# Performance work log

Hardware: AMD Instinct MI355X
Metric: run time of the kernel (lower is better)

## Reference

```python
import jax
jax.config.update("jax_enable_x64", True)
import jax.numpy as jnp
import numpy as np

B = 32768   # batch size
V = 256     # number of label variables (chain junction tree, C = V-1 pairwise cliques)


def setup_inputs() -> dict:
    key = jax.random.key(0)
    k1, k2 = jax.random.split(key)
    fs = jax.random.normal(k1, (B, V), dtype=jnp.float32)
    labels = jax.random.randint(k2, (B,), 0, V, dtype=jnp.int64)
    return {"fs": fs, "labels": labels}


def _hex_loss(fs, labels):
    # eTable = fs.T / numVar  (numVar[v] = number of cliques containing v: 2 interior, 1 endpoints)
    e = fs.astype(jnp.float64).T  # (V, B)
    numVar = jnp.concatenate([jnp.ones((1,)), 2.0 * jnp.ones((V - 2,)), jnp.ones((1,))]).astype(jnp.float64)
    e = e / numVar[:, None]
    a, b = e[:-1], e[1:]                      # (C, B) per-clique unary terms for (v_i, v_{i+1})
    s = jnp.array([0.0, 1.0], dtype=jnp.float64)
    # assignPotential: pot[c, s0, s1, :] = exp(stateSpace @ eTable[vars_c])
    pot = jnp.exp(s[None, :, None, None] * a[:, None, None, :]
                  + s[None, None, :, None] * b[:, None, None, :])  # (C, 2, 2, B)

    init = jnp.ones((2, B), dtype=jnp.float64)

    # upward pass: message into clique c from the left over shared var v_c
    def fwd_step(carry, p):
        new = jnp.einsum('ijb,ib->jb', p, carry)
        return new, carry
    _, alphas = jax.lax.scan(fwd_step, init, pot)   # (C, 2, B), alphas[c] = msg from clique c-1

    # downward pass: message into clique c from the right over shared var v_{c+1}
    def bwd_step(carry, p):
        new = jnp.einsum('ijb,jb->ib', p, carry)
        return new, carry
    _, betas = jax.lax.scan(bwd_step, init, pot, reverse=True)  # (C, 2, B), betas[c] = msg from clique c+1

    # clique beliefs = potential * prod(incoming messages)
    bel = pot * alphas[:, :, None, :] * betas[:, None, :, :]  # (C, 2, 2, B)
    z = bel[0].sum(axis=(0, 1))                               # (B,) partition fn from root clique

    # marginal P(y_v = 1): sum belief rows with v set to 1 in its clique
    pm_head = bel[:, 1, :, :].sum(axis=1)       # (C, B) vars 0..V-2 (position s0 of clique v)
    pm_last = bel[-1, :, 1, :].sum(axis=0)      # (B,)  var V-1 (position s1 of last clique)
    pMargin = jnp.concatenate([pm_head, pm_last[None]], axis=0) / z  # (V, B)

    sel = jnp.take_along_axis(pMargin, labels[None, :], axis=0)[0]   # (B,)
    valid = (sel > 0) & (z > 0) & jnp.isfinite(z)
    loss_i = jnp.where(valid, -jnp.log(jnp.where(valid, sel, 1.0)), 0.0)
    return jnp.mean(loss_i)


def reference(fs, labels):
    return _hex_loss(fs, labels)
```

## Files before the change

### kernel.cpp

```cpp
#include <hip/hip_runtime.h>


#ifndef HEX_B
#define HEX_B 32768
#endif
#ifndef HEX_V
#define HEX_V 256
#endif

__global__ void hex_partial_kernel(const float* __restrict__ fs,
                                   const int* __restrict__ labels,
                                   double* __restrict__ partial,
                                   int Bn, int Vn) {
    __shared__ double sdata[256];
    const int tid = threadIdx.x;
    const int stride = gridDim.x * blockDim.x;
    double s = 0.0;
    for (int b = blockIdx.x * blockDim.x + tid; b < Bn; b += stride) {
        const int lab = labels[b];
        const double x = (double)fs[(size_t)b * (size_t)Vn + (size_t)lab];
        const double l = (x > 0.0) ? log1p(exp(-x)) : (-x + log1p(exp(x)));
        s += l;
    }
    sdata[tid] = s;
    __syncthreads();
    for (int off = blockDim.x >> 1; off > 0; off >>= 1) {
        if (tid < off) sdata[tid] += sdata[tid + off];
        __syncthreads();
    }
    if (tid == 0) partial[blockIdx.x] = sdata[0];
}

__global__ void hex_final_kernel(const double* __restrict__ partial,
                                 int nblocks,
                                 float* __restrict__ out,
                                 int Bn) {
    __shared__ double sdata[256];
    const int tid = threadIdx.x;
    double s = 0.0;
    for (int i = tid; i < nblocks; i += blockDim.x) s += partial[i];
    sdata[tid] = s;
    __syncthreads();
    for (int off = blockDim.x >> 1; off > 0; off >>= 1) {
        if (tid < off) sdata[tid] += sdata[tid + off];
        __syncthreads();
    }
    if (tid == 0) out[0] = (float)(sdata[0] / (double)Bn);
}

extern "C" void kernel_launch(void* const* d_in, const int* in_sizes, int n_in,
                              void* d_out, int out_size, void* d_ws, size_t ws_size,
                              hipStream_t stream) {
    const float* fs = (const float*)d_in[0];
    const int* labels = (const int*)d_in[1];
    float* out = (float*)d_out;

    const int Bn = in_sizes[1];
    const int Vn = in_sizes[0] / Bn;

    const int threads = 256;
    const int blocks = 128;
    double* partial = (double*)d_ws;

    hex_partial_kernel<<<blocks, threads, 0, stream>>>(fs, labels, partial, Bn, Vn);
    hex_final_kernel<<<1, threads, 0, stream>>>(partial, blocks, out, Bn);
}
```

Before: 11.47 us.

## Fuse partial and final reductions into one cooperative kernel with float math

Merges the two launches into a single cooperative kernel that uses a grid-wide sync before block 0 sums the per-block partials. It also moves the per-element softplus and the in-block reduction from double to float, and launches one thread per batch element instead of a grid-stride loop over 128 blocks. The aim is to drop a kernel launch and cut the cost of fp64 transcendentals. In exchange it adds the overhead of a cooperative launch and a grid barrier, and slightly lowers accumulation precision.

```diff
diff --git a/kernel.cpp b/kernel.cpp
--- a/kernel.cpp
+++ b/kernel.cpp
@@ -1,51 +1,47 @@
 #include <hip/hip_runtime.h>
+#include <hip/hip_cooperative_groups.h>
+
+namespace cg = cooperative_groups;
 
 
-#ifndef HEX_B
-#define HEX_B 32768
-#endif
-#ifndef HEX_V
-#define HEX_V 256
-#endif
+__global__ void hex_fused_kernel(const float* __restrict__ fs,
+                                 const int* __restrict__ labels,
+                                 double* __restrict__ partial,
+                                 float* __restrict__ out,
+                                 int Bn, int Vn) {
+    __shared__ float sdata[256];
+    __shared__ double ddata[256];
 
-__global__ void hex_partial_kernel(const float* __restrict__ fs,
-                                   const int* __restrict__ labels,
-                                   double* __restrict__ partial,
-                                   int Bn, int Vn) {
-    __shared__ double sdata[256];
     const int tid = threadIdx.x;
-    const int stride = gridDim.x * blockDim.x;
-    double s = 0.0;
-    for (int b = blockIdx.x * blockDim.x + tid; b < Bn; b += stride) {
+    const int b = blockIdx.x * blockDim.x + tid;
+
+    float l = 0.0f;
+    if (b < Bn) {
         const int lab = labels[b];
-        const double x = (double)fs[(size_t)b * (size_t)Vn + (size_t)lab];
-        const double l = (x > 0.0) ? log1p(exp(-x)) : (-x + log1p(exp(x)));
-        s += l;
+        const float x = fs[(size_t)b * (size_t)Vn + (size_t)lab];
+        l = (x > 0.0f) ? log1pf(expf(-x)) : (-x + log1pf(expf(x)));
     }
-    sdata[tid] = s;
+    sdata[tid] = l;
     __syncthreads();
     for (int off = blockDim.x >> 1; off > 0; off >>= 1) {
         if (tid < off) sdata[tid] += sdata[tid + off];
         __syncthreads();
     }
-    if (tid == 0) partial[blockIdx.x] = sdata[0];
-}
+    if (tid == 0) partial[blockIdx.x] = (double)sdata[0];
 
-__global__ void hex_final_kernel(const double* __restrict__ partial,
-                                 int nblocks,
-                                 float* __restrict__ out,
-                                 int Bn) {
-    __shared__ double sdata[256];
-    const int tid = threadIdx.x;
-    double s = 0.0;
-    for (int i = tid; i < nblocks; i += blockDim.x) s += partial[i];
-    sdata[tid] = s;
-    __syncthreads();
-    for (int off = blockDim.x >> 1; off > 0; off >>= 1) {
-        if (tid < off) sdata[tid] += sdata[tid + off];
+    cg::this_grid().sync();
+
+    if (blockIdx.x == 0) {
+        double s = 0.0;
+        for (int i = tid; i < gridDim.x; i += blockDim.x) s += partial[i];
+        ddata[tid] = s;
         __syncthreads();
+        for (int off = blockDim.x >> 1; off > 0; off >>= 1) {
+            if (tid < off) ddata[tid] += ddata[tid + off];
+            __syncthreads();
+        }
+        if (tid == 0) out[0] = (float)(ddata[0] / (double)Bn);
     }
-    if (tid == 0) out[0] = (float)(sdata[0] / (double)Bn);
 }
 
 extern "C" void kernel_launch(void* const* d_in, const int* in_sizes, int n_in,
@@ -55,13 +51,15 @@
     const int* labels = (const int*)d_in[1];
     float* out = (float*)d_out;
 
-    const int Bn = in_sizes[1];
-    const int Vn = in_sizes[0] / Bn;
-
-    const int threads = 256;
-    const int blocks = 128;
+    int Bn = in_sizes[1];
+    int Vn = in_sizes[0] / Bn;
     double* partial = (double*)d_ws;
 
-    hex_partial_kernel<<<blocks, threads, 0, stream>>>(fs, labels, partial, Bn, Vn);
-    hex_final_kernel<<<1, threads, 0, stream>>>(partial, blocks, out, Bn);
+    int threads = 256;
+    int blocks = (Bn + threads - 1) / threads;
+
+    void* args[] = {(void*)&fs, (void*)&labels, (void*)&partial,
+                    (void*)&out, (void*)&Bn, (void*)&Vn};
+    hipLaunchCooperativeKernel((const void*)hex_fused_kernel,
+                               dim3(blocks), dim3(threads), args, 0, stream);
 }
```

Result: slower. 39.00 us (+240.1%).
